# Optimization experiments

Measured on AMD Instinct MI355X. Metric: run time of the kernel, lower is better.

## Reference

```python
import jax, jax.numpy as jnp
import numpy as np

NUM_GRAPHS = 64
NEG_SLOPE = 0.2


def gat_layer(x, src, dst, W, a_src, a_dst, b, concat):
    # x: [N, F_in], W: [F_in, H*C], a_src/a_dst: [H, C], b: [H*C] or [C]
    N = x.shape[0]
    H, C = a_src.shape
    h = (x @ W).reshape(N, H, C)                      # [N, H, C]
    alpha_src = jnp.sum(h * a_src[None], axis=-1)     # [N, H]
    alpha_dst = jnp.sum(h * a_dst[None], axis=-1)     # [N, H]
    e = alpha_src[src] + alpha_dst[dst]               # [E, H]
    e = jax.nn.leaky_relu(e, NEG_SLOPE)
    # segment softmax over incoming edges of each dst node
    m = jax.ops.segment_max(e, dst, num_segments=N)   # [N, H]
    ex = jnp.exp(e - m[dst])
    s = jax.ops.segment_sum(ex, dst, num_segments=N)  # [N, H]
    alpha = ex / (s[dst] + 1e-16)                     # [E, H]
    msg = h[src] * alpha[:, :, None]                  # [E, H, C]
    out = jax.ops.segment_sum(msg, dst, num_segments=N)  # [N, H, C]
    if concat:
        out = out.reshape(N, H * C)
    else:
        out = out.mean(axis=1)
    return out + b


def setup_inputs() -> dict:
    key = jax.random.key(0)
    ks = jax.random.split(key, 12)
    N, E, F_in, Hd, Out, H = 50000, 400000, 128, 64, 64, 8
    x = jax.random.normal(ks[0], (N, F_in), dtype=jnp.float32)
    edge_index = jax.random.randint(ks[1], (2, E), 0, N, dtype=jnp.int64)
    batch = jnp.sort(jax.random.randint(ks[2], (N,), 0, NUM_GRAPHS, dtype=jnp.int64))
    s1 = 1.0 / np.sqrt(F_in)
    W1 = jax.random.normal(ks[3], (F_in, H * Hd), dtype=jnp.float32) * s1
    a_src1 = jax.random.normal(ks[4], (H, Hd), dtype=jnp.float32) * 0.1
    a_dst1 = jax.random.normal(ks[5], (H, Hd), dtype=jnp.float32) * 0.1
    b1 = jnp.zeros((H * Hd,), dtype=jnp.float32)
    s2 = 1.0 / np.sqrt(H * Hd)
    W2 = jax.random.normal(ks[6], (H * Hd, H * Out), dtype=jnp.float32) * s2
    a_src2 = jax.random.normal(ks[7], (H, Out), dtype=jnp.float32) * 0.1
    a_dst2 = jax.random.normal(ks[8], (H, Out), dtype=jnp.float32) * 0.1
    b2 = jnp.zeros((Out,), dtype=jnp.float32)
    return {"x": x, "edge_index": edge_index, "batch": batch,
            "W1": W1, "a_src1": a_src1, "a_dst1": a_dst1, "b1": b1,
            "W2": W2, "a_src2": a_src2, "a_dst2": a_dst2, "b2": b2}


def reference(x, edge_index, batch, W1, a_src1, a_dst1, b1, W2, a_src2, a_dst2, b2):
    N = x.shape[0]
    # add self-loops (PyG GATConv default add_self_loops=True)
    loop = jnp.arange(N, dtype=edge_index.dtype)
    src = jnp.concatenate([edge_index[0], loop])
    dst = jnp.concatenate([edge_index[1], loop])
    h = jax.nn.elu(gat_layer(x, src, dst, W1, a_src1, a_dst1, b1, concat=True))
    h = jax.nn.elu(gat_layer(h, src, dst, W2, a_src2, a_dst2, b2, concat=False))
    # global mean pool over graphs
    sums = jax.ops.segment_sum(h, batch, num_segments=NUM_GRAPHS)
    cnts = jax.ops.segment_sum(jnp.ones((N,), h.dtype), batch, num_segments=NUM_GRAPHS)
    return sums / jnp.maximum(cnts, 1.0)[:, None]
```

## Files before the change

### kernel.cpp

```cpp
#include <hip/hip_runtime.h>
#include <hip/hip_bf16.h>
#include <hip/hip_fp16.h>
#include <math.h>

#define NN   50000
#define NE   400000
#define NET  450000
#define FH   8
#define FC   64
#define FHC  512
#define FIN  128
#define NG   64
#define MPAD 50048
#define CAP  64

typedef unsigned short u16;
typedef _Float16 f16x8 __attribute__((ext_vector_type(8)));
typedef float f32x4 __attribute__((ext_vector_type(4)));
typedef unsigned short u16x8 __attribute__((ext_vector_type(8)));

static __device__ __forceinline__ u16 f2h(float f) {
  return __half_as_ushort(__float2half(f));
}
static __device__ __forceinline__ float h2f(u16 u) {
  return __half2float(__ushort_as_half(u));
}

#define R0 (NN * FIN / 4)
#define R1 (FIN * FHC)
#define R2 (FHC * FHC)
#define R3 ((MPAD - NN) * FIN / 8)
#define R4 ((MPAD - NN) * FHC / 8)
#define R5 (NN / 4)
#define R6 (2 * NG)
#define PREP_T (R0 + R1 + R2 + R3 + R4 + R5 + R6)

__global__ __launch_bounds__(256) void prep_k(const float* __restrict__ x,
                                              const float* __restrict__ W1,
                                              const float* __restrict__ W2,
                                              u16* __restrict__ xf,
                                              u16* __restrict__ w1t,
                                              u16* __restrict__ w2t,
                                              u16* __restrict__ h1f,
                                              int* __restrict__ cnt,
                                              int* __restrict__ gse) {
  int t = blockIdx.x * 256 + threadIdx.x;
  if (t < R0) {
    float4 f = reinterpret_cast<const float4*>(x)[t];
    ushort4 h;
    h.x = f2h(f.x); h.y = f2h(f.y); h.z = f2h(f.z); h.w = f2h(f.w);
    reinterpret_cast<ushort4*>(xf)[t] = h;
    return;
  }
  t -= R0;
  if (t < R1) {
    int k = t >> 9, n = t & 511;
    w1t[n * FIN + k] = f2h(W1[t]);
    return;
  }
  t -= R1;
  if (t < R2) {
    int k = t >> 9, n = t & 511;
    w2t[n * FHC + k] = f2h(W2[t]);
    return;
  }
  t -= R2;
  if (t < R3) {
    reinterpret_cast<u16x8*>(xf + (size_t)NN * FIN)[t] = (u16x8)0;
    return;
  }
  t -= R3;
  if (t < R4) {
    reinterpret_cast<u16x8*>(h1f + (size_t)NN * FHC)[t] = (u16x8)0;
    return;
  }
  t -= R4;
  if (t < R5) {
    reinterpret_cast<int4*>(cnt)[t] = make_int4(0, 0, 0, 0);
    return;
  }
  t -= R5;
  if (t < R6) gse[t] = 0;
}

__global__ __launch_bounds__(256) void gemm_mfma(const u16* __restrict__ Af,
                                                 const u16* __restrict__ Bf,
                                                 u16* __restrict__ Cb,
                                                 const float* __restrict__ As_g,
                                                 const float* __restrict__ Ad_g,
                                                 float* __restrict__ asrc,
                                                 float* __restrict__ adst,
                                                 int M, int K) {
  constexpr int BK = 32;
  __shared__ u16 As[128 * BK];
  __shared__ u16 Bs[128 * BK];
  const int tid = threadIdx.x;
  constexpr int NWG = (MPAD / 128) * (FHC / 128);
  constexpr int qq = NWG >> 3, rr = NWG & 7;
  int d = blockIdx.x;
  int xcd = d & 7, slot = d >> 3;
  int w = (xcd < rr) ? xcd * (qq + 1) + slot
                     : rr * (qq + 1) + (xcd - rr) * qq + slot;
  const int bm = (w >> 2) * 128;
  const int bn = (w & 3) * 128;
  const int wv = tid >> 6, l = tid & 63;
  const int wr = wv >> 1, wc = wv & 1;
  const int fr = l & 15, fq = l >> 4;

  f32x4 acc[4][4] = {};

  for (int k0 = 0; k0 < K; k0 += BK) {
    __syncthreads();
#pragma unroll
    for (int i = 0; i < 2; ++i) {
      int idx = i * 256 + tid;
      int row = idx >> 2, c8 = idx & 3;
      size_t goA = (size_t)(bm + row) * K + k0 + c8 * 8;
      size_t goB = (size_t)(bn + row) * K + k0 + c8 * 8;
      __builtin_amdgcn_global_load_lds(
          (const __attribute__((address_space(1))) void*)(Af + goA),
          (__attribute__((address_space(3))) void*)(As + idx * 8), 16, 0, 0);
      __builtin_amdgcn_global_load_lds(
          (const __attribute__((address_space(1))) void*)(Bf + goB),
          (__attribute__((address_space(3))) void*)(Bs + idx * 8), 16, 0, 0);
    }
    __syncthreads();
    {
      f16x8 av[4], bv[4];
#pragma unroll
      for (int mi = 0; mi < 4; ++mi)
        av[mi] = *reinterpret_cast<const f16x8*>(
            As + (wr * 64 + mi * 16 + fr) * BK + fq * 8);
#pragma unroll
      for (int ni = 0; ni < 4; ++ni)
        bv[ni] = *reinterpret_cast<const f16x8*>(
            Bs + (wc * 64 + ni * 16 + fr) * BK + fq * 8);
#pragma unroll
      for (int mi = 0; mi < 4; ++mi)
#pragma unroll
        for (int ni = 0; ni < 4; ++ni)
          acc[mi][ni] = __builtin_amdgcn_mfma_f32_16x16x32_f16(
              av[mi], bv[ni], acc[mi][ni], 0, 0, 0);
    }
  }
#pragma unroll
  for (int mi = 0; mi < 4; ++mi)
#pragma unroll
    for (int ni = 0; ni < 4; ++ni) {
      int r0 = bm + wr * 64 + mi * 16 + fq * 4;
      int c0 = bn + wc * 64 + ni * 16 + fr;
#pragma unroll
      for (int j = 0; j < 4; ++j)
        if (r0 + j < M) Cb[(size_t)(r0 + j) * FHC + c0] = f2h(acc[mi][ni][j]);
    }
  {
    int hd = (bn >> 6) + wc;
    int cb = bn + wc * 64 + fr;
    float as_v[4], ad_v[4];
#pragma unroll
    for (int ni = 0; ni < 4; ++ni) {
      as_v[ni] = As_g[cb + ni * 16];
      ad_v[ni] = Ad_g[cb + ni * 16];
    }
#pragma unroll
    for (int mi = 0; mi < 4; ++mi)
#pragma unroll
      for (int j = 0; j < 4; ++j) {
        float ps = 0.f, pd = 0.f;
#pragma unroll
        for (int ni = 0; ni < 4; ++ni) {
          float v = acc[mi][ni][j];
          ps += v * as_v[ni];
          pd += v * ad_v[ni];
        }
#pragma unroll
        for (int off = 1; off < 16; off <<= 1) {
          ps += __shfl_xor(ps, off);
          pd += __shfl_xor(pd, off);
        }
        int row = bm + wr * 64 + mi * 16 + fq * 4 + j;
        if (fr == 0 && row < M) {
          asrc[row * FH + hd] = ps;
          adst[row * FH + hd] = pd;
        }
      }
  }
}

__global__ __launch_bounds__(256) void fillbnd_k(const int* __restrict__ ei,
                                                 int* __restrict__ cnt,
                                                 int* __restrict__ col,
                                                 const int* __restrict__ batch,
                                                 int* __restrict__ gstart,
                                                 int* __restrict__ gend) {
  int t = blockIdx.x * 256 + threadIdx.x;
  if (t < NET) {
    int s, d;
    if (t < NE) { s = ei[t]; d = ei[NE + t]; } else { s = d = t - NE; }
    int pos = atomicAdd(&cnt[d], 1);
    if (pos < CAP) col[((size_t)d << 6) + pos] = s;
    return;
  }
  int n = t - NET;
  if (n >= NN) return;
  int b = batch[n];
  if (n == 0 || batch[n - 1] != b) gstart[b] = n;
  if (n == NN - 1 || batch[n + 1] != b) gend[b] = n + 1;
}

template <int LAYER>
__global__ __launch_bounds__(256) void gather_k(const int* __restrict__ cntp,
                                                const int* __restrict__ col,
                                                const float* __restrict__ asrc,
                                                const float* __restrict__ adst,
                                                const u16* __restrict__ hb,
                                                const float* __restrict__ bias,
                                                u16* __restrict__ outb,
                                                float* __restrict__ nodeval) {
  int n = blockIdx.x * 4 + (threadIdx.x >> 6);
  if (n >= NN) return;
  int lane = threadIdx.x & 63;
  int hh = lane & 7;
  int hsel = lane >> 3;
  int cnt = cntp[n];
  const int* cb = col + ((size_t)n << 6);
  float adn = adst[n * FH + hh];
  float den = 0.f;
  float v[8] = {};
  for (int j0 = 0; j0 < cnt; j0 += 4) {
    int sidx[4];
#pragma unroll
    for (int u = 0; u < 4; ++u) {
      int jj = (j0 + u < cnt) ? j0 + u : cnt - 1;
      sidx[u] = cb[jj];
    }
    float ex[4];
#pragma unroll
    for (int u = 0; u < 4; ++u) {
      float el = asrc[sidx[u] * FH + hh] + adn;
      el = el > 0.f ? el : 0.2f * el;
      ex[u] = (j0 + u < cnt) ? __expf(el) : 0.f;
      den += ex[u];
    }
    u16x8 hv[4];
#pragma unroll
    for (int u = 0; u < 4; ++u)
      hv[u] = *reinterpret_cast<const u16x8*>(hb + (size_t)sidx[u] * FHC + lane * 8);
#pragma unroll
    for (int u = 0; u < 4; ++u) {
      float exv = __shfl(ex[u], hsel);
#pragma unroll
      for (int j = 0; j < 8; ++j) v[j] += exv * h2f(hv[u][j]);
    }
  }
  float dh = __shfl(den, hsel);
  float inv = 1.f / (dh + 1e-16f);
#pragma unroll
  for (int j = 0; j < 8; ++j) v[j] *= inv;
  if (LAYER == 1) {
    const float4* bp = reinterpret_cast<const float4*>(bias + lane * 8);
    float4 b0 = bp[0], b1 = bp[1];
    float bb[8] = {b0.x, b0.y, b0.z, b0.w, b1.x, b1.y, b1.z, b1.w};
    u16x8 ov;
#pragma unroll
    for (int j = 0; j < 8; ++j) {
      float val = v[j] + bb[j];
      val = val > 0.f ? val : expm1f(val);
      ov[j] = f2h(val);
    }
    *reinterpret_cast<u16x8*>(outb + (size_t)n * FHC + lane * 8) = ov;
  } else {
#pragma unroll
    for (int off = 8; off < 64; off <<= 1)
#pragma unroll
      for (int j = 0; j < 8; ++j) v[j] += __shfl_xor(v[j], off);
    if (lane < 8) {
      const float4* bp = reinterpret_cast<const float4*>(bias + lane * 8);
      float4 b0 = bp[0], b1 = bp[1];
      float bb[8] = {b0.x, b0.y, b0.z, b0.w, b1.x, b1.y, b1.z, b1.w};
      float o[8];
#pragma unroll
      for (int j = 0; j < 8; ++j) {
        float val = v[j] * (1.f / FH) + bb[j];
        o[j] = val > 0.f ? val : expm1f(val);
      }
      float4* np = reinterpret_cast<float4*>(nodeval + (size_t)n * FC + lane * 8);
      np[0] = make_float4(o[0], o[1], o[2], o[3]);
      np[1] = make_float4(o[4], o[5], o[6], o[7]);
    }
  }
}

__global__ __launch_bounds__(256) void pool_k(const float* __restrict__ nodeval,
                                              const int* __restrict__ gstart,
                                              const int* __restrict__ gend,
                                              float* __restrict__ out) {
  __shared__ float red[4][FC];
  int g = blockIdx.x;
  int c = threadIdx.x & 63, w = threadIdx.x >> 6;
  int s = gstart[g], e = gend[g];
  float acc = 0.f;
  for (int n = s + w; n < e; n += 4) acc += nodeval[(size_t)n * FC + c];
  red[w][c] = acc;
  __syncthreads();
  if (w == 0) {
    float v = red[0][c] + red[1][c] + red[2][c] + red[3][c];
    out[g * FC + c] = v / fmaxf((float)(e - s), 1.f);
  }
}

extern "C" void kernel_launch(void* const* d_in, const int* in_sizes, int n_in,
                              void* d_out, int out_size, void* d_ws, size_t ws_size,
                              hipStream_t stream) {
  const float* x    = (const float*)d_in[0];
  const int*   ei   = (const int*)d_in[1];
  const int*   batch= (const int*)d_in[2];
  const float* W1   = (const float*)d_in[3];
  const float* as1  = (const float*)d_in[4];
  const float* ad1  = (const float*)d_in[5];
  const float* b1   = (const float*)d_in[6];
  const float* W2   = (const float*)d_in[7];
  const float* as2  = (const float*)d_in[8];
  const float* ad2  = (const float*)d_in[9];
  const float* b2   = (const float*)d_in[10];
  float* out = (float*)d_out;

  char* p = (char*)d_ws;
  u16* Cb  = (u16*)p; p += (size_t)NN * FHC * 2;
  u16* xf  = (u16*)p; p += (size_t)MPAD * FIN * 2;
  u16* h1f = (u16*)p; p += (size_t)MPAD * FHC * 2;
  u16* w1t = (u16*)p; p += (size_t)FHC * FIN * 2;
  u16* w2t = (u16*)p; p += (size_t)FHC * FHC * 2;
  float* asrc = (float*)p;            p += (size_t)NN * FH * 4;
  float* adst = (float*)p;            p += (size_t)NN * FH * 4;
  int* cnt    = (int*)p;              p += (size_t)NN * 4;
  int* col    = (int*)p;              p += (size_t)NN * CAP * 4;
  int* gse    = (int*)p;              p += (size_t)NG * 2 * 4;
  int* gstart = gse;
  int* gend   = gse + NG;
  float* nodeval = (float*)xf;

  const int NWG = (MPAD / 128) * (FHC / 128);
  const int ngrid = (NN + 3) / 4;

  prep_k<<<(PREP_T + 255) / 256, 256, 0, stream>>>(x, W1, W2, xf, w1t, w2t,
                                                   h1f, cnt, gse);

  fillbnd_k<<<(NET + NN + 255) / 256, 256, 0, stream>>>(ei, cnt, col,
                                                        batch, gstart, gend);

  gemm_mfma<<<NWG, 256, 0, stream>>>(xf, w1t, Cb, as1, ad1, asrc, adst, NN, FIN);
  gather_k<1><<<ngrid, 256, 0, stream>>>(cnt, col, asrc, adst, Cb, b1,
                                         h1f, nullptr);

  gemm_mfma<<<NWG, 256, 0, stream>>>(h1f, w2t, Cb, as2, ad2, asrc, adst, NN, FHC);
  gather_k<2><<<ngrid, 256, 0, stream>>>(cnt, col, asrc, adst, Cb, b2,
                                         nullptr, nodeval);

  pool_k<<<NG, 256, 0, stream>>>(nodeval, gstart, gend, out);
}
```

Measured before the change: 326.3 us.

## Double-buffer GEMM LDS tiles and coalesce weight transpose writes

The MFMA GEMM now keeps two LDS buffers for the A and B tiles. It issues the async global-to-LDS loads for the next K step before computing on the current one, which leaves one barrier per iteration instead of two. This is meant to hide global load latency behind the MFMA work, at the cost of twice the LDS per block, which may lower occupancy. Separately, the weight transpose-and-convert loops now index by output element, so stores are contiguous and reads are strided.

```diff
diff --git a/kernel.cpp b/kernel.cpp
--- a/kernel.cpp
+++ b/kernel.cpp
@@ -54,14 +54,14 @@
   }
   t -= R0;
   if (t < R1) {
-    int k = t >> 9, n = t & 511;
-    w1t[n * FIN + k] = f2h(W1[t]);
+    int n = t >> 7, k = t & 127;
+    w1t[t] = f2h(W1[k * FHC + n]);
     return;
   }
   t -= R1;
   if (t < R2) {
-    int k = t >> 9, n = t & 511;
-    w2t[n * FHC + k] = f2h(W2[t]);
+    int n = t >> 9, k = t & 511;
+    w2t[t] = f2h(W2[k * FHC + n]);
     return;
   }
   t -= R2;
@@ -92,8 +92,8 @@
                                                  float* __restrict__ adst,
                                                  int M, int K) {
   constexpr int BK = 32;
-  __shared__ u16 As[128 * BK];
-  __shared__ u16 Bs[128 * BK];
+  __shared__ u16 As[2][128 * BK];
+  __shared__ u16 Bs[2][128 * BK];
   const int tid = threadIdx.x;
   constexpr int NWG = (MPAD / 128) * (FHC / 128);
   constexpr int qq = NWG >> 3, rr = NWG & 7;
@@ -107,41 +107,58 @@
   const int wr = wv >> 1, wc = wv & 1;
   const int fr = l & 15, fq = l >> 4;
 
-  f32x4 acc[4][4] = {};
-
-  for (int k0 = 0; k0 < K; k0 += BK) {
-    __syncthreads();
-#pragma unroll
-    for (int i = 0; i < 2; ++i) {
-      int idx = i * 256 + tid;
-      int row = idx >> 2, c8 = idx & 3;
-      size_t goA = (size_t)(bm + row) * K + k0 + c8 * 8;
-      size_t goB = (size_t)(bn + row) * K + k0 + c8 * 8;
+  const int sidx0 = tid, sidx1 = 256 + tid;
+  const int srow0 = sidx0 >> 2, sc80 = sidx0 & 3;
+  const int srow1 = sidx1 >> 2, sc81 = sidx1 & 3;
+
+  auto stage = [&](int buf, int k0) {
+    {
+      size_t goA = (size_t)(bm + srow0) * K + k0 + sc80 * 8;
+      size_t goB = (size_t)(bn + srow0) * K + k0 + sc80 * 8;
       __builtin_amdgcn_global_load_lds(
           (const __attribute__((address_space(1))) void*)(Af + goA),
-          (__attribute__((address_space(3))) void*)(As + idx * 8), 16, 0, 0);
+          (__attribute__((address_space(3))) void*)(As[buf] + sidx0 * 8), 16, 0, 0);
       __builtin_amdgcn_global_load_lds(
           (const __attribute__((address_space(1))) void*)(Bf + goB),
-          (__attribute__((address_space(3))) void*)(Bs + idx * 8), 16, 0, 0);
-    }
+          (__attribute__((address_space(3))) void*)(Bs[buf] + sidx0 * 8), 16, 0, 0);
+    }
+    {
+      size_t goA = (size_t)(bm + srow1) * K + k0 + sc81 * 8;
+      size_t goB = (size_t)(bn + srow1) * K + k0 + sc81 * 8;
+      __builtin_amdgcn_global_load_lds(
+          (const __attribute__((address_space(1))) void*)(Af + goA),
+          (__attribute__((address_space(3))) void*)(As[buf] + sidx1 * 8), 16, 0, 0);
+      __builtin_amdgcn_global_load_lds(
+          (const __attribute__((address_space(1))) void*)(Bf + goB),
+          (__attribute__((address_space(3))) void*)(Bs[buf] + sidx1 * 8), 16, 0, 0);
+    }
+  };
+
+  f32x4 acc[4][4] = {};
+
+  stage(0, 0);
+  __syncthreads();
+  int cur = 0;
+  const int nt = K / BK;
+  for (int t = 0; t < nt; ++t) {
+    if (t + 1 < nt) stage(cur ^ 1, (t + 1) * BK);
+    f16x8 av[4], bv[4];
+#pragma unroll
+    for (int mi = 0; mi < 4; ++mi)
+      av[mi] = *reinterpret_cast<const f16x8*>(
+          As[cur] + (wr * 64 + mi * 16 + fr) * BK + fq * 8);
+#pragma unroll
+    for (int ni = 0; ni < 4; ++ni)
+      bv[ni] = *reinterpret_cast<const f16x8*>(
+          Bs[cur] + (wc * 64 + ni * 16 + fr) * BK + fq * 8);
+#pragma unroll
+    for (int mi = 0; mi < 4; ++mi)
+#pragma unroll
+      for (int ni = 0; ni < 4; ++ni)
+        acc[mi][ni] = __builtin_amdgcn_mfma_f32_16x16x32_f16(
+            av[mi], bv[ni], acc[mi][ni], 0, 0, 0);
     __syncthreads();
-    {
-      f16x8 av[4], bv[4];
-#pragma unroll
-      for (int mi = 0; mi < 4; ++mi)
-        av[mi] = *reinterpret_cast<const f16x8*>(
-            As + (wr * 64 + mi * 16 + fr) * BK + fq * 8);
-#pragma unroll
-      for (int ni = 0; ni < 4; ++ni)
-        bv[ni] = *reinterpret_cast<const f16x8*>(
-            Bs + (wc * 64 + ni * 16 + fr) * BK + fq * 8);
-#pragma unroll
-      for (int mi = 0; mi < 4; ++mi)
-#pragma unroll
-        for (int ni = 0; ni < 4; ++ni)
-          acc[mi][ni] = __builtin_amdgcn_mfma_f32_16x16x32_f16(
-              av[mi], bv[ni], acc[mi][ni], 0, 0, 0);
-    }
+    cur ^= 1;
   }
 #pragma unroll
   for (int mi = 0; mi < 4; ++mi)
```

After: 323.3 us. No clear change (-0.9%).
